# Optimization experiments

Hardware: AMD Instinct MI355X
Metric: run time of the kernel (lower is better)

The kernel has to match this reference:

```python
import jax, jax.numpy as jnp
import numpy as np

N_NODES = 50000
N_EDGES = 800000
IN_DIM = 128
HID = 128
TIME = 6.0
STEPS = 12


def setup_inputs() -> dict:
    key = jax.random.key(0)
    ks = jax.random.split(key, 8)
    gat_out = jax.random.normal(ks[0], (N_NODES, IN_DIM), dtype=jnp.float32)
    edge_index = jax.random.randint(ks[1], (2, N_EDGES), 0, N_NODES, dtype=jnp.int64)
    # scale weights like PyTorch Linear default (uniform-ish magnitude)
    W_in = jax.random.normal(ks[2], (IN_DIM, HID), dtype=jnp.float32) * (1.0 / np.sqrt(IN_DIM))
    b_in = jnp.zeros((HID,), dtype=jnp.float32)
    W1 = jax.random.normal(ks[3], (HID, 2 * HID), dtype=jnp.float32) * (1.0 / np.sqrt(HID))
    b1 = jnp.zeros((2 * HID,), dtype=jnp.float32)
    W2 = jax.random.normal(ks[4], (2 * HID, HID), dtype=jnp.float32) * (1.0 / np.sqrt(2 * HID))
    b2 = jnp.zeros((HID,), dtype=jnp.float32)
    clearance = jnp.full((1,), 0.1, dtype=jnp.float32)
    return {"gat_out": gat_out, "edge_index": edge_index, "W_in": W_in, "b_in": b_in,
            "W1": W1, "b1": b1, "W2": W2, "b2": b2, "clearance": clearance}


def reference(gat_out, edge_index, W_in, b_in, W1, b1, W2, b2, clearance):
    N = gat_out.shape[0]
    dt = TIME / STEPS
    src, dst = edge_index[0], edge_index[1]
    h = jnp.tanh(gat_out @ W_in + b_in)  # [N, HID]
    # degree is identical each Euler step in the original; hoist it once
    deg = jax.ops.segment_sum(jnp.ones((src.shape[0],), dtype=h.dtype), dst, num_segments=N)
    deg = jnp.clip(deg, 1.0, None)[:, None]  # [N, 1]
    decay = jax.nn.relu(clearance)  # [1]

    def step(h, _):
        agg = jax.ops.segment_sum(h[src], dst, num_segments=N) / deg  # [N, HID]
        diff = jnp.tanh(jax.nn.gelu(agg @ W1 + b1, approximate=False) @ W2 + b2)
        h = h + (diff - decay * h) * dt
        return h, None

    h, _ = jax.lax.scan(step, h, None, length=STEPS)
    return h
```

## Files before the change

kernel.cpp:

```cpp
#include <hip/hip_runtime.h>
#include <math.h>

#define N_NODES 50000
#define N_EDGES 800000
#define HID 128
#define H2 256
#define STEPS 12
#define DT 0.5f

#define SCAN_B 256
#define NB ((N_NODES + SCAN_B - 1) / SCAN_B)
#define NODE_BLOCKS ((N_NODES + 31) / 32)
#define N_PAD (NODE_BLOCKS * 32)
#define CSR_CAP (N_EDGES + 8 * N_NODES)

typedef __attribute__((ext_vector_type(8))) short bf16x8;
typedef __attribute__((ext_vector_type(4))) float f32x4;

__device__ inline unsigned short f2bf(float x) {
    unsigned int u = __float_as_uint(x);
    unsigned int r = (u + 0x7FFFu + ((u >> 16) & 1u)) >> 16;
    return (unsigned short)r;
}
__device__ inline float bf2f(unsigned short b) {
    return __uint_as_float(((unsigned int)b) << 16);
}
__device__ inline float u2f(unsigned int u) { return __uint_as_float(u); }

__device__ inline float fast_tanh(float x) {
    float xc = fminf(fmaxf(x, -9.0f), 9.0f);
    float t = __builtin_amdgcn_exp2f(xc * 2.8853900817779268f);
    return 1.0f - 2.0f * __builtin_amdgcn_rcpf(t + 1.0f);
}

__device__ inline float fast_gelu(float x) {
    float u  = x * 0.70710678118654752f;
    float au = fabsf(u);
    float t  = __builtin_amdgcn_rcpf(fmaf(0.3275911f, au, 1.0f));
    float poly = t * (0.254829592f + t * (-0.284496736f + t * (1.421413741f +
                 t * (-1.453152027f + t * 1.061405429f))));
    float ex = __builtin_amdgcn_exp2f(-au * au * 1.4426950408889634f);
    float erfv = copysignf(1.0f - poly * ex, u);
    return 0.5f * x * (1.0f + erfv);
}


__global__ void k_init(int* __restrict__ counts,
                       unsigned short* __restrict__ a, unsigned short* __restrict__ b) {
    int i = blockIdx.x * 256 + threadIdx.x;
    if (i < N_NODES) counts[i] = 0;
    if (i < (N_PAD - N_NODES) * HID) {
        a[(size_t)N_NODES * HID + i] = 0;
        b[(size_t)N_NODES * HID + i] = 0;
    }
}

__global__ void k_hist(const int* __restrict__ dst, int* __restrict__ counts) {
    int e = blockIdx.x * 256 + threadIdx.x;
    if (e < N_EDGES) atomicAdd(&counts[dst[e]], 1);
}

__global__ void k_blocksum(const int* __restrict__ counts, int* __restrict__ bsum) {
    __shared__ int s[SCAN_B];
    int idx = blockIdx.x * SCAN_B + threadIdx.x;
    int v = (idx < N_NODES) ? ((counts[idx] + 7) & ~7) : 0;
    s[threadIdx.x] = v;
    __syncthreads();
    for (int off = SCAN_B / 2; off > 0; off >>= 1) {
        if (threadIdx.x < off) s[threadIdx.x] += s[threadIdx.x + off];
        __syncthreads();
    }
    if (threadIdx.x == 0) bsum[blockIdx.x] = s[0];
}

__global__ void k_scan_bsums(int* __restrict__ bsum, int* __restrict__ offsets) {
    __shared__ int s[SCAN_B];
    int tid = threadIdx.x;
    int v = (tid < NB) ? bsum[tid] : 0;
    s[tid] = v;
    __syncthreads();
    for (int off = 1; off < SCAN_B; off <<= 1) {
        int t = 0;
        if (tid >= off) t = s[tid - off];
        __syncthreads();
        s[tid] += t;
        __syncthreads();
    }
    if (tid < NB) bsum[tid] = s[tid] - v;
    if (tid == SCAN_B - 1) offsets[N_NODES] = s[SCAN_B - 1];
}

__global__ void k_offsets(const int* __restrict__ counts, const int* __restrict__ bsum,
                          int* __restrict__ offsets, int* __restrict__ cursor,
                          int* __restrict__ csr_src) {
    __shared__ int s[SCAN_B];
    int idx = blockIdx.x * SCAN_B + threadIdx.x;
    int d = (idx < N_NODES) ? counts[idx] : 0;
    int v = (d + 7) & ~7;
    s[threadIdx.x] = v;
    __syncthreads();
    for (int off = 1; off < SCAN_B; off <<= 1) {
        int t = 0;
        if ((int)threadIdx.x >= off) t = s[threadIdx.x - off];
        __syncthreads();
        s[threadIdx.x] += t;
        __syncthreads();
    }
    if (idx < N_NODES) {
        int excl = s[threadIdx.x] - v;
        int o = bsum[blockIdx.x] + excl;
        offsets[idx] = o;
        cursor[idx]  = o;
        for (int j = d; j < v; j++) csr_src[o + j] = N_NODES;
    }
}

__global__ void k_scatter(const int* __restrict__ src, const int* __restrict__ dst,
                          int* __restrict__ cursor, int* __restrict__ csr_src) {
    int e = blockIdx.x * 256 + threadIdx.x;
    if (e < N_EDGES) {
        int d = dst[e];
        int p = atomicAdd(&cursor[d], 1);
        csr_src[p] = src[e];
    }
}


__global__ void k_pack_all(const float* __restrict__ W1, const float* __restrict__ W2,
                           const float* __restrict__ Win,
                           unsigned short* __restrict__ w1h, unsigned short* __restrict__ w2h,
                           unsigned short* __restrict__ winh) {
    int t = blockIdx.x * 256 + threadIdx.x;
    int tile = t >> 6, l = t & 63;
    const float* W; unsigned short* out; int K, N, ti;
    if (tile < 64)       { W = W1;  out = w1h;  K = 128; N = 256; ti = tile; }
    else if (tile < 128) { W = W2;  out = w2h;  K = 256; N = 128; ti = tile - 64; }
    else if (tile < 160) { W = Win; out = winh; K = 128; N = 128; ti = tile - 128; }
    else return;
    int KT = K >> 5;
    int kt = ti % KT, nt = ti / KT;
    int n  = nt * 16 + (l & 15);
    int k0 = kt * 32 + (l >> 4) * 8;
    int base = ((nt * KT + kt) * 64 + l) * 8;
    for (int j = 0; j < 8; j++)
        out[base + j] = f2bf(W[(size_t)(k0 + j) * N + n]);
}


__global__ __launch_bounds__(256, 3) void k_h0_mfma(
    const float* __restrict__ gat,
    const unsigned short* __restrict__ wh,
    const float* __restrict__ b_in, float* __restrict__ h,
    unsigned short* __restrict__ hbf) {
    __shared__ unsigned short Ahi[32][136];
    __shared__ unsigned short Alo[32][136];
    int tid = threadIdx.x;
    int node0 = blockIdx.x * 32;

    for (int idx = tid; idx < 32 * 64; idx += 256) {
        int m = idx >> 6, c = (idx & 63) * 2;
        float2 v;
        if (node0 + m < N_NODES) v = *(const float2*)&gat[(size_t)(node0 + m) * 128 + c];
        else { v.x = 0.f; v.y = 0.f; }
        unsigned short h0 = f2bf(v.x), h1 = f2bf(v.y);
        unsigned short l0 = f2bf(v.x - bf2f(h0)), l1 = f2bf(v.y - bf2f(h1));
        *(unsigned int*)&Ahi[m][c] = (unsigned int)h0 | ((unsigned int)h1 << 16);
        *(unsigned int*)&Alo[m][c] = (unsigned int)l0 | ((unsigned int)l1 << 16);
    }
    __syncthreads();

    int l = tid & 63, wv = tid >> 6;
    int c15 = l & 15, q = l >> 4;
    f32x4 acc[2][2] = {};
#pragma unroll
    for (int kt = 0; kt < 4; kt++) {
        bf16x8 ah[2], al[2];
#pragma unroll
        for (int mt = 0; mt < 2; mt++) {
            ah[mt] = *(const bf16x8*)&Ahi[mt * 16 + c15][kt * 32 + q * 8];
            al[mt] = *(const bf16x8*)&Alo[mt * 16 + c15][kt * 32 + q * 8];
        }
#pragma unroll
        for (int nn = 0; nn < 2; nn++) {
            int nt = wv * 2 + nn;
            bf16x8 bh = *(const bf16x8*)&wh[(size_t)((nt * 4 + kt) * 64 + l) * 8];
#pragma unroll
            for (int mt = 0; mt < 2; mt++) {
                acc[mt][nn] = __builtin_amdgcn_mfma_f32_16x16x32_bf16(ah[mt], bh, acc[mt][nn], 0, 0, 0);
                acc[mt][nn] = __builtin_amdgcn_mfma_f32_16x16x32_bf16(al[mt], bh, acc[mt][nn], 0, 0, 0);
            }
        }
    }
#pragma unroll
    for (int nn = 0; nn < 2; nn++) {
        int col = (wv * 2 + nn) * 16 + c15;
        float bb = b_in[col];
#pragma unroll
        for (int mt = 0; mt < 2; mt++)
#pragma unroll
            for (int r = 0; r < 4; r++) {
                int node = node0 + mt * 16 + q * 4 + r;
                if (node < N_NODES) {
                    float v = fast_tanh(acc[mt][nn][r] + bb);
                    h[(size_t)node * 128 + col]   = v;
                    hbf[(size_t)node * 128 + col] = f2bf(v);
                }
            }
    }
}


#define ACC8(V) \
    a0 += u2f((V).x << 16); a1 += u2f((V).x & 0xFFFF0000u); \
    a2 += u2f((V).y << 16); a3 += u2f((V).y & 0xFFFF0000u); \
    a4 += u2f((V).z << 16); a5 += u2f((V).z & 0xFFFF0000u); \
    a6 += u2f((V).w << 16); a7 += u2f((V).w & 0xFFFF0000u);

__global__ __launch_bounds__(512, 4) void k_step(
    const unsigned short* __restrict__ hbf_in,
    float* __restrict__ h, unsigned short* __restrict__ hbf_out,
    const int* __restrict__ offsets, const int* __restrict__ csr,
    const int* __restrict__ cnt,
    const unsigned short* __restrict__ w1h,
    const float* __restrict__ b1,
    const unsigned short* __restrict__ w2h,
    const float* __restrict__ b2, const float* __restrict__ clr) {
    __shared__ unsigned short Ahi[32][136];
    __shared__ unsigned short Alo[32][136];
    __shared__ unsigned short Y[32][264];
    int tid = threadIdx.x, l = tid & 63, wv = tid >> 6;
    int c15 = l & 15, q = l >> 4;
    int node0 = blockIdx.x * 32;
    int g  = l >> 4;
    int cl = l & 15;

    {
        int m = wv * 4 + g;
        int node = node0 + m;
        float a0 = 0.f, a1 = 0.f, a2 = 0.f, a3 = 0.f;
        float a4 = 0.f, a5 = 0.f, a6 = 0.f, a7 = 0.f;
        int deg = 0;
        if (node < N_NODES) {
            deg = cnt[node];
            int beg = offsets[node];
            int end = beg + ((deg + 7) & ~7);
            const unsigned short* hb = hbf_in + cl * 8;
            if (beg < end) {
                int4 i0 = *(const int4*)&csr[beg];
                int4 i1 = *(const int4*)&csr[beg + 4];
                for (int e = beg; e < end; e += 8) {
                    int enx = (e + 8 < end) ? (e + 8) : e;
                    int4 j0 = *(const int4*)&csr[enx];
                    int4 j1 = *(const int4*)&csr[enx + 4];
                    uint4 w0 = *(const uint4*)&hb[((unsigned)i0.x) << 7];
                    uint4 w1 = *(const uint4*)&hb[((unsigned)i0.y) << 7];
                    uint4 w2 = *(const uint4*)&hb[((unsigned)i0.z) << 7];
                    uint4 w3 = *(const uint4*)&hb[((unsigned)i0.w) << 7];
                    uint4 w4 = *(const uint4*)&hb[((unsigned)i1.x) << 7];
                    uint4 w5 = *(const uint4*)&hb[((unsigned)i1.y) << 7];
                    uint4 w6 = *(const uint4*)&hb[((unsigned)i1.z) << 7];
                    uint4 w7 = *(const uint4*)&hb[((unsigned)i1.w) << 7];
                    i0 = j0; i1 = j1;
                    ACC8(w0); ACC8(w1); ACC8(w2); ACC8(w3);
                    ACC8(w4); ACC8(w5); ACC8(w6); ACC8(w7);
                }
            }
        }
        float inv = (deg > 1) ? 1.0f / (float)deg : 1.0f;
        float x0 = a0 * inv, x1 = a1 * inv, x2 = a2 * inv, x3 = a3 * inv;
        float x4 = a4 * inv, x5 = a5 * inv, x6 = a6 * inv, x7 = a7 * inv;
        unsigned short h0 = f2bf(x0), h1 = f2bf(x1), h2 = f2bf(x2), h3 = f2bf(x3);
        unsigned short h4 = f2bf(x4), h5 = f2bf(x5), h6 = f2bf(x6), h7 = f2bf(x7);
        uint4 ohi;
        ohi.x = (unsigned int)h0 | ((unsigned int)h1 << 16);
        ohi.y = (unsigned int)h2 | ((unsigned int)h3 << 16);
        ohi.z = (unsigned int)h4 | ((unsigned int)h5 << 16);
        ohi.w = (unsigned int)h6 | ((unsigned int)h7 << 16);
        *(uint4*)&Ahi[m][cl * 8] = ohi;
        unsigned short l0 = f2bf(x0 - bf2f(h0)), l1 = f2bf(x1 - bf2f(h1));
        unsigned short l2 = f2bf(x2 - bf2f(h2)), l3 = f2bf(x3 - bf2f(h3));
        unsigned short l4 = f2bf(x4 - bf2f(h4)), l5 = f2bf(x5 - bf2f(h5));
        unsigned short l6 = f2bf(x6 - bf2f(h6)), l7 = f2bf(x7 - bf2f(h7));
        uint4 olo;
        olo.x = (unsigned int)l0 | ((unsigned int)l1 << 16);
        olo.y = (unsigned int)l2 | ((unsigned int)l3 << 16);
        olo.z = (unsigned int)l4 | ((unsigned int)l5 << 16);
        olo.w = (unsigned int)l6 | ((unsigned int)l7 << 16);
        *(uint4*)&Alo[m][cl * 8] = olo;
    }
    __syncthreads();

    {
        f32x4 acc1[2][2] = {};
#pragma unroll
        for (int kt = 0; kt < 4; kt++) {
            bf16x8 ah[2], al[2];
#pragma unroll
            for (int mt = 0; mt < 2; mt++) {
                ah[mt] = *(const bf16x8*)&Ahi[mt * 16 + c15][kt * 32 + q * 8];
                al[mt] = *(const bf16x8*)&Alo[mt * 16 + c15][kt * 32 + q * 8];
            }
#pragma unroll
            for (int nn = 0; nn < 2; nn++) {
                int nt = wv * 2 + nn;
                bf16x8 bh = *(const bf16x8*)&w1h[(size_t)((nt * 4 + kt) * 64 + l) * 8];
#pragma unroll
                for (int mt = 0; mt < 2; mt++) {
                    acc1[mt][nn] = __builtin_amdgcn_mfma_f32_16x16x32_bf16(ah[mt], bh, acc1[mt][nn], 0, 0, 0);
                    acc1[mt][nn] = __builtin_amdgcn_mfma_f32_16x16x32_bf16(al[mt], bh, acc1[mt][nn], 0, 0, 0);
                }
            }
        }
#pragma unroll
        for (int nn = 0; nn < 2; nn++) {
            int col = (wv * 2 + nn) * 16 + c15;
            float bb = b1[col];
#pragma unroll
            for (int mt = 0; mt < 2; mt++)
#pragma unroll
                for (int r = 0; r < 4; r++) {
                    int row = mt * 16 + q * 4 + r;
                    float x = acc1[mt][nn][r] + bb;
                    Y[row][col] = f2bf(fast_gelu(x));
                }
        }
    }
    __syncthreads();

    f32x4 acc2[2] = {};
#pragma unroll
    for (int kt = 0; kt < 8; kt++) {
        bf16x8 ya[2];
#pragma unroll
        for (int mt = 0; mt < 2; mt++)
            ya[mt] = *(const bf16x8*)&Y[mt * 16 + c15][kt * 32 + q * 8];
        bf16x8 bh = *(const bf16x8*)&w2h[(size_t)((wv * 8 + kt) * 64 + l) * 8];
#pragma unroll
        for (int mt = 0; mt < 2; mt++)
            acc2[mt] = __builtin_amdgcn_mfma_f32_16x16x32_bf16(ya[mt], bh, acc2[mt], 0, 0, 0);
    }
    float decay = fmaxf(clr[0], 0.0f);
    {
        int col = wv * 16 + c15;
        float bb = b2[col];
#pragma unroll
        for (int mt = 0; mt < 2; mt++)
#pragma unroll
            for (int r = 0; r < 4; r++) {
                int node = node0 + mt * 16 + q * 4 + r;
                if (node < N_NODES) {
                    float hv = h[(size_t)node * 128 + col];
                    float diff = fast_tanh(acc2[mt][r] + bb);
                    float nh = hv + (diff - decay * hv) * DT;
                    h[(size_t)node * 128 + col]       = nh;
                    hbf_out[(size_t)node * 128 + col] = f2bf(nh);
                }
            }
    }
}


extern "C" void kernel_launch(void* const* d_in, const int* in_sizes, int n_in,
                              void* d_out, int out_size, void* d_ws, size_t ws_size,
                              hipStream_t stream) {
    const float* gat   = (const float*)d_in[0];
    const int*   edges = (const int*)d_in[1];
    const float* W_in  = (const float*)d_in[2];
    const float* b_in  = (const float*)d_in[3];
    const float* W1    = (const float*)d_in[4];
    const float* b1    = (const float*)d_in[5];
    const float* W2    = (const float*)d_in[6];
    const float* b2    = (const float*)d_in[7];
    const float* clr   = (const float*)d_in[8];
    float* h = (float*)d_out;

    const int* src = edges;
    const int* dst = edges + N_EDGES;

    char* ws = (char*)d_ws;
    size_t off = 0;
    auto alloc = [&](size_t bytes) -> void* {
        off = (off + 255) & ~(size_t)255;
        void* p = ws + off;
        off += bytes;
        return p;
    };
    int*   counts  = (int*)alloc(sizeof(int) * N_NODES);
    int*   offsets = (int*)alloc(sizeof(int) * (N_NODES + 1));
    int*   cursor  = (int*)alloc(sizeof(int) * N_NODES);
    int*   bsum    = (int*)alloc(sizeof(int) * NB);
    int*   csr_src = (int*)alloc(sizeof(int) * CSR_CAP);
    unsigned short* hbfA = (unsigned short*)alloc(sizeof(short) * (size_t)N_PAD * HID);
    unsigned short* hbfB = (unsigned short*)alloc(sizeof(short) * (size_t)N_PAD * HID);
    unsigned short* w1h  = (unsigned short*)alloc(sizeof(short) * HID * H2);
    unsigned short* w2h  = (unsigned short*)alloc(sizeof(short) * H2 * HID);
    unsigned short* winh = (unsigned short*)alloc(sizeof(short) * HID * HID);

    k_pack_all<<<40, 256, 0, stream>>>(W1, W2, W_in, w1h, w2h, winh);

    k_init<<<NB, 256, 0, stream>>>(counts, hbfA, hbfB);
    k_hist<<<(N_EDGES + 255) / 256, 256, 0, stream>>>(dst, counts);
    k_blocksum<<<NB, 256, 0, stream>>>(counts, bsum);
    k_scan_bsums<<<1, SCAN_B, 0, stream>>>(bsum, offsets);
    k_offsets<<<NB, 256, 0, stream>>>(counts, bsum, offsets, cursor, csr_src);
    k_scatter<<<(N_EDGES + 255) / 256, 256, 0, stream>>>(src, dst, cursor, csr_src);

    k_h0_mfma<<<NODE_BLOCKS, 256, 0, stream>>>(gat, winh, b_in, h, hbfA);

    for (int s = 0; s < STEPS; s++) {
        const unsigned short* in = (s & 1) ? hbfB : hbfA;
        unsigned short*      out = (s & 1) ? hbfA : hbfB;
        k_step<<<NODE_BLOCKS, 512, 0, stream>>>(in, h, out, offsets, csr_src, counts,
                                                w1h, b1, w2h, b2, clr);
    }
}
```

Baseline: 772.0 us.

## Sort nodes by degree within tiles and replace scan with atomic offsets

Adds a per-32-node-tile rank kernel that permutes nodes by in-degree, so wavefront groups in the step kernel gather neighbours with similar loop trip counts and diverge less. The three-kernel prefix scan for CSR offsets is replaced by a single atomic-bump allocation, and weight packing is folded into the init kernel, cutting launches. The cost is an extra perm indirection per node access in every step and non-contiguous CSR placement.

```diff
diff --git a/kernel.cpp b/kernel.cpp
--- a/kernel.cpp
+++ b/kernel.cpp
@@ -8,8 +8,7 @@
 #define STEPS 12
 #define DT 0.5f
 
-#define SCAN_B 256
-#define NB ((N_NODES + SCAN_B - 1) / SCAN_B)
+#define NB ((N_NODES + 255) / 256)
 #define NODE_BLOCKS ((N_NODES + 31) / 32)
 #define N_PAD (NODE_BLOCKS * 32)
 #define CSR_CAP (N_EDGES + 8 * N_NODES)
@@ -45,14 +44,33 @@
 }
 
 
-__global__ void k_init(int* __restrict__ counts,
-                       unsigned short* __restrict__ a, unsigned short* __restrict__ b) {
+__global__ void k_init(int* __restrict__ counts, int* __restrict__ gcur,
+                       unsigned short* __restrict__ a, unsigned short* __restrict__ b,
+                       const float* __restrict__ W1, const float* __restrict__ W2,
+                       const float* __restrict__ Win,
+                       unsigned short* __restrict__ w1h, unsigned short* __restrict__ w2h,
+                       unsigned short* __restrict__ winh) {
     int i = blockIdx.x * 256 + threadIdx.x;
+    if (i == 0) *gcur = 0;
     if (i < N_NODES) counts[i] = 0;
     if (i < (N_PAD - N_NODES) * HID) {
         a[(size_t)N_NODES * HID + i] = 0;
         b[(size_t)N_NODES * HID + i] = 0;
     }
+    int tile = i >> 6, l = i & 63;
+    if (tile < 160) {
+        const float* W; unsigned short* out; int K, N, ti;
+        if (tile < 64)       { W = W1;  out = w1h;  K = 128; N = 256; ti = tile; }
+        else if (tile < 128) { W = W2;  out = w2h;  K = 256; N = 128; ti = tile - 64; }
+        else                 { W = Win; out = winh; K = 128; N = 128; ti = tile - 128; }
+        int KT = K >> 5;
+        int kt = ti % KT, nt = ti / KT;
+        int n  = nt * 16 + (l & 15);
+        int k0 = kt * 32 + (l >> 4) * 8;
+        int base = ((nt * KT + kt) * 64 + l) * 8;
+        for (int j = 0; j < 8; j++)
+            out[base + j] = f2bf(W[(size_t)(k0 + j) * N + n]);
+    }
 }
 
 __global__ void k_hist(const int* __restrict__ dst, int* __restrict__ counts) {
@@ -60,58 +78,38 @@
     if (e < N_EDGES) atomicAdd(&counts[dst[e]], 1);
 }
 
-__global__ void k_blocksum(const int* __restrict__ counts, int* __restrict__ bsum) {
-    __shared__ int s[SCAN_B];
-    int idx = blockIdx.x * SCAN_B + threadIdx.x;
-    int v = (idx < N_NODES) ? ((counts[idx] + 7) & ~7) : 0;
-    s[threadIdx.x] = v;
+
+__global__ void k_rank(const int* __restrict__ counts, int* __restrict__ perm) {
+    __shared__ int sd[256];
+    int t = threadIdx.x;
+    int sub = t >> 5, lane = t & 31;
+    int tile = blockIdx.x * 8 + sub;
+    int node = tile * 32 + lane;
+    int deg = (tile < NODE_BLOCKS && node < N_NODES) ? counts[node] : 0x7FFFFFFF;
+    sd[t] = deg;
     __syncthreads();
-    for (int off = SCAN_B / 2; off > 0; off >>= 1) {
-        if (threadIdx.x < off) s[threadIdx.x] += s[threadIdx.x + off];
-        __syncthreads();
-    }
-    if (threadIdx.x == 0) bsum[blockIdx.x] = s[0];
-}
-
-__global__ void k_scan_bsums(int* __restrict__ bsum, int* __restrict__ offsets) {
-    __shared__ int s[SCAN_B];
-    int tid = threadIdx.x;
-    int v = (tid < NB) ? bsum[tid] : 0;
-    s[tid] = v;
-    __syncthreads();
-    for (int off = 1; off < SCAN_B; off <<= 1) {
-        int t = 0;
-        if (tid >= off) t = s[tid - off];
-        __syncthreads();
-        s[tid] += t;
-        __syncthreads();
-    }
-    if (tid < NB) bsum[tid] = s[tid] - v;
-    if (tid == SCAN_B - 1) offsets[N_NODES] = s[SCAN_B - 1];
-}
-
-__global__ void k_offsets(const int* __restrict__ counts, const int* __restrict__ bsum,
-                          int* __restrict__ offsets, int* __restrict__ cursor,
-                          int* __restrict__ csr_src) {
-    __shared__ int s[SCAN_B];
-    int idx = blockIdx.x * SCAN_B + threadIdx.x;
-    int d = (idx < N_NODES) ? counts[idx] : 0;
-    int v = (d + 7) & ~7;
-    s[threadIdx.x] = v;
-    __syncthreads();
-    for (int off = 1; off < SCAN_B; off <<= 1) {
-        int t = 0;
-        if ((int)threadIdx.x >= off) t = s[threadIdx.x - off];
-        __syncthreads();
-        s[threadIdx.x] += t;
-        __syncthreads();
-    }
-    if (idx < N_NODES) {
-        int excl = s[threadIdx.x] - v;
-        int o = bsum[blockIdx.x] + excl;
-        offsets[idx] = o;
-        cursor[idx]  = o;
-        for (int j = d; j < v; j++) csr_src[o + j] = N_NODES;
+    if (tile < NODE_BLOCKS) {
+        int base = sub * 32;
+        int r = 0;
+        for (int j = 0; j < 32; j++) {
+            int dj = sd[base + j];
+            r += (dj < deg) || (dj == deg && j < lane);
+        }
+        perm[tile * 32 + r] = node;
+    }
+}
+
+__global__ void k_offsets_atomic(const int* __restrict__ counts, int* __restrict__ gcur,
+                                 int* __restrict__ offsets, int* __restrict__ cursor,
+                                 int* __restrict__ csr_src) {
+    int i = blockIdx.x * 256 + threadIdx.x;
+    if (i < N_NODES) {
+        int d = counts[i];
+        int p = (d + 7) & ~7;
+        int o = atomicAdd(gcur, p);
+        offsets[i] = o;
+        cursor[i]  = o;
+        for (int j = d; j < p; j++) csr_src[o + j] = N_NODES;
     }
 }
 
@@ -123,27 +121,6 @@
         int p = atomicAdd(&cursor[d], 1);
         csr_src[p] = src[e];
     }
-}
-
-
-__global__ void k_pack_all(const float* __restrict__ W1, const float* __restrict__ W2,
-                           const float* __restrict__ Win,
-                           unsigned short* __restrict__ w1h, unsigned short* __restrict__ w2h,
-                           unsigned short* __restrict__ winh) {
-    int t = blockIdx.x * 256 + threadIdx.x;
-    int tile = t >> 6, l = t & 63;
-    const float* W; unsigned short* out; int K, N, ti;
-    if (tile < 64)       { W = W1;  out = w1h;  K = 128; N = 256; ti = tile; }
-    else if (tile < 128) { W = W2;  out = w2h;  K = 256; N = 128; ti = tile - 64; }
-    else if (tile < 160) { W = Win; out = winh; K = 128; N = 128; ti = tile - 128; }
-    else return;
-    int KT = K >> 5;
-    int kt = ti % KT, nt = ti / KT;
-    int n  = nt * 16 + (l & 15);
-    int k0 = kt * 32 + (l >> 4) * 8;
-    int base = ((nt * KT + kt) * 64 + l) * 8;
-    for (int j = 0; j < 8; j++)
-        out[base + j] = f2bf(W[(size_t)(k0 + j) * N + n]);
 }
 
 
@@ -220,7 +197,7 @@
     const unsigned short* __restrict__ hbf_in,
     float* __restrict__ h, unsigned short* __restrict__ hbf_out,
     const int* __restrict__ offsets, const int* __restrict__ csr,
-    const int* __restrict__ cnt,
+    const int* __restrict__ cnt, const int* __restrict__ perm,
     const unsigned short* __restrict__ w1h,
     const float* __restrict__ b1,
     const unsigned short* __restrict__ w2h,
@@ -236,7 +213,7 @@
 
     {
         int m = wv * 4 + g;
-        int node = node0 + m;
+        int node = perm[node0 + m];
         float a0 = 0.f, a1 = 0.f, a2 = 0.f, a3 = 0.f;
         float a4 = 0.f, a5 = 0.f, a6 = 0.f, a7 = 0.f;
         int deg = 0;
@@ -347,7 +324,8 @@
         for (int mt = 0; mt < 2; mt++)
 #pragma unroll
             for (int r = 0; r < 4; r++) {
-                int node = node0 + mt * 16 + q * 4 + r;
+                int row = mt * 16 + q * 4 + r;
+                int node = perm[node0 + row];
                 if (node < N_NODES) {
                     float hv = h[(size_t)node * 128 + col];
                     float diff = fast_tanh(acc2[mt][r] + bb);
@@ -386,9 +364,10 @@
         return p;
     };
     int*   counts  = (int*)alloc(sizeof(int) * N_NODES);
-    int*   offsets = (int*)alloc(sizeof(int) * (N_NODES + 1));
+    int*   offsets = (int*)alloc(sizeof(int) * N_NODES);
     int*   cursor  = (int*)alloc(sizeof(int) * N_NODES);
-    int*   bsum    = (int*)alloc(sizeof(int) * NB);
+    int*   perm    = (int*)alloc(sizeof(int) * N_PAD);
+    int*   gcur    = (int*)alloc(sizeof(int));
     int*   csr_src = (int*)alloc(sizeof(int) * CSR_CAP);
     unsigned short* hbfA = (unsigned short*)alloc(sizeof(short) * (size_t)N_PAD * HID);
     unsigned short* hbfB = (unsigned short*)alloc(sizeof(short) * (size_t)N_PAD * HID);
@@ -396,13 +375,11 @@
     unsigned short* w2h  = (unsigned short*)alloc(sizeof(short) * H2 * HID);
     unsigned short* winh = (unsigned short*)alloc(sizeof(short) * HID * HID);
 
-    k_pack_all<<<40, 256, 0, stream>>>(W1, W2, W_in, w1h, w2h, winh);
-
-    k_init<<<NB, 256, 0, stream>>>(counts, hbfA, hbfB);
+    k_init<<<NB, 256, 0, stream>>>(counts, gcur, hbfA, hbfB,
+                                   W1, W2, W_in, w1h, w2h, winh);
     k_hist<<<(N_EDGES + 255) / 256, 256, 0, stream>>>(dst, counts);
-    k_blocksum<<<NB, 256, 0, stream>>>(counts, bsum);
-    k_scan_bsums<<<1, SCAN_B, 0, stream>>>(bsum, offsets);
-    k_offsets<<<NB, 256, 0, stream>>>(counts, bsum, offsets, cursor, csr_src);
+    k_rank<<<(NODE_BLOCKS + 7) / 8, 256, 0, stream>>>(counts, perm);
+    k_offsets_atomic<<<NB, 256, 0, stream>>>(counts, gcur, offsets, cursor, csr_src);
     k_scatter<<<(N_EDGES + 255) / 256, 256, 0, stream>>>(src, dst, cursor, csr_src);
 
     k_h0_mfma<<<NODE_BLOCKS, 256, 0, stream>>>(gat, winh, b_in, h, hbfA);
@@ -410,7 +387,7 @@
     for (int s = 0; s < STEPS; s++) {
         const unsigned short* in = (s & 1) ? hbfB : hbfA;
         unsigned short*      out = (s & 1) ? hbfA : hbfB;
-        k_step<<<NODE_BLOCKS, 512, 0, stream>>>(in, h, out, offsets, csr_src, counts,
+        k_step<<<NODE_BLOCKS, 512, 0, stream>>>(in, h, out, offsets, csr_src, counts, perm,
                                                 w1h, b1, w2h, b2, clr);
     }
 }
```

Result: slower. 821.7 us (+6.4%).
